# Kernel tuning notes

Measured on AMD Instinct MI355X. Metric: run time of the kernel, lower is better.

## Reference

```python
import jax, jax.numpy as jnp
import numpy as np

N, E, F, H, G = 50000, 1600000, 128, 128, 64
EPS = 1e-5  # BatchNorm eps


def setup_inputs() -> dict:
    key = jax.random.key(0)
    ks = jax.random.split(key, 16)
    x = jax.random.normal(ks[0], (N, F), dtype=jnp.float32)
    edge_index = jax.random.randint(ks[1], (2, E), 0, N, dtype=jnp.int64)
    batch = jnp.sort(jax.random.randint(ks[2], (N,), 0, G, dtype=jnp.int64))
    inp = {
        'x': x, 'edge_index': edge_index, 'batch': batch,
        'W1': jax.random.normal(ks[3], (F, H), dtype=jnp.float32) / np.sqrt(F),
        'b1': jnp.zeros((H,), jnp.float32),
        'bn1_gamma': jax.random.uniform(ks[4], (H,), jnp.float32, 0.5, 1.5),
        'bn1_beta': jax.random.normal(ks[5], (H,), jnp.float32) * 0.1,
        'bn1_mean': jax.random.normal(ks[6], (H,), jnp.float32) * 0.1,
        'bn1_var': jax.random.uniform(ks[7], (H,), jnp.float32, 0.5, 1.5),
        'W2': jax.random.normal(ks[8], (H, H), dtype=jnp.float32) / np.sqrt(H),
        'b2': jnp.zeros((H,), jnp.float32),
        'bn2_gamma': jax.random.uniform(ks[9], (H,), jnp.float32, 0.5, 1.5),
        'bn2_beta': jax.random.normal(ks[10], (H,), jnp.float32) * 0.1,
        'bn2_mean': jax.random.normal(ks[11], (H,), jnp.float32) * 0.1,
        'bn2_var': jax.random.uniform(ks[12], (H,), jnp.float32, 0.5, 1.5),
        'att_w': jax.random.normal(ks[13], (H, 1), dtype=jnp.float32) / np.sqrt(H),
        'cls_w': jax.random.normal(ks[14], (1, H), dtype=jnp.float32) / np.sqrt(H),
        'cls_b': jnp.zeros((1,), jnp.float32),
    }
    return inp


def gcn_conv(h, W, b, src, dst, n):
    # PyG GCNConv: linear, add self-loops, symmetric D^{-1/2}(A+I)D^{-1/2} aggregation, bias.
    hw = h @ W                                   # [n, H]
    loops = jnp.arange(n, dtype=src.dtype)
    s = jnp.concatenate([src, loops])
    d = jnp.concatenate([dst, loops])
    deg = jax.ops.segment_sum(jnp.ones_like(d, dtype=hw.dtype), d, num_segments=n)
    dis = jnp.where(deg > 0, jax.lax.rsqrt(deg), 0.0)
    norm = dis[s] * dis[d]                       # [E+n]
    msgs = hw[s] * norm[:, None]                 # gather + scale (memory-bound)
    return jax.ops.segment_sum(msgs, d, num_segments=n) + b


def batch_norm(h, gamma, beta, mean, var):
    return (h - mean) * gamma * jax.lax.rsqrt(var + EPS) + beta


def reference(x, edge_index, batch, W1, b1, bn1_gamma, bn1_beta, bn1_mean, bn1_var,
              W2, b2, bn2_gamma, bn2_beta, bn2_mean, bn2_var, att_w, cls_w, cls_b):
    n = x.shape[0]
    src, dst = edge_index[0], edge_index[1]
    # eval mode: dropout and edge-dropout are no-ops; BN uses running stats
    h = gcn_conv(x, W1, b1, src, dst, n)
    h = jax.nn.relu(batch_norm(h, bn1_gamma, bn1_beta, bn1_mean, bn1_var))
    h = gcn_conv(h, W2, b2, src, dst, n)
    h = jax.nn.relu(batch_norm(h, bn2_gamma, bn2_beta, bn2_mean, bn2_var))
    att = jax.nn.sigmoid(h @ att_w)              # [n, 1]
    g = jax.ops.segment_sum(h * att, batch, num_segments=G)  # [G, H]
    logits = g @ cls_w.T + cls_b                 # [G, 1]
    return logits, att
```

## Files before the change

kernel.cpp:

```cpp
#include <hip/hip_runtime.h>
#include <math.h>

#define NN 50000
#define HID 128
#define NG 64
#define BN_EPS 1e-5f

typedef __attribute__((ext_vector_type(8))) short short8;
typedef __attribute__((ext_vector_type(4))) float f32x4;

__device__ inline unsigned pack_bf2(float a, float b) {
    union { float f; unsigned u; } ua, ub;
    ua.f = a; ub.f = b;
    unsigned x = ua.u, y = ub.u;
    x += 0x7fffu + ((x >> 16) & 1u);
    y += 0x7fffu + ((y >> 16) & 1u);
    return (x >> 16) | (y & 0xffff0000u);
}
__device__ inline unsigned short bf16_1(float x) {
    union { float f; unsigned u; } v;
    v.f = x;
    unsigned r = v.u + 0x7fffu + ((v.u >> 16) & 1u);
    return (unsigned short)(r >> 16);
}
__device__ inline float2 unpack_bf2(unsigned v) {
    union { unsigned u; float f; } a, b;
    a.u = v << 16;
    b.u = v & 0xffff0000u;
    return make_float2(a.f, b.f);
}

#define NBKT 256
#define ETILE 2048
#define EPT   (ETILE / 256)
#define CAP   8192
#define ASTR 136

__global__ __launch_bounds__(128) void k_prep0(const float* __restrict__ W1,
                                               const float* __restrict__ W2,
                                               unsigned short* __restrict__ wt1,
                                               unsigned short* __restrict__ wt2,
                                               int* __restrict__ bcurP,
                                               const float* __restrict__ cls_b,
                                               float* __restrict__ logits) {
    int b = blockIdx.x;
    int t = threadIdx.x;
    if (b < 256) {
        int k = b & 127;
        const float* W = (b < 128) ? W1 : W2;
        unsigned short* wt = (b < 128) ? wt1 : wt2;
        wt[t * 128 + k] = bf16_1(W[k * 128 + t]);
    } else {
        #pragma unroll
        for (int i = 0; i < 32; ++i) bcurP[t * 32 + i] = 0;
        if (t < NG) logits[t] = cls_b[0];
    }
}

__global__ __launch_bounds__(256) void k_distribute(const int* __restrict__ src,
                                                    const int* __restrict__ dst,
                                                    int* __restrict__ bcurP,
                                                    unsigned* __restrict__ bpacked,
                                                    int E, int K) {
    __shared__ int h[NBKT];
    __shared__ int sx[NBKT];
    __shared__ int cur[NBKT];
    __shared__ int gb[NBKT];
    __shared__ unsigned stage[ETILE];
    int t = threadIdx.x;
    h[t] = 0;
    __syncthreads();
    int base = blockIdx.x * ETILE;
    int dreg[EPT];
    #pragma unroll
    for (int i = 0; i < EPT; ++i) {
        int e = base + i * 256 + t;
        dreg[i] = (e < E) ? dst[e] : -1;
        if (dreg[i] >= 0) atomicAdd(&h[dreg[i] / K], 1);
    }
    __syncthreads();
    int c = h[t];
    sx[t] = c;
    __syncthreads();
    for (int off = 1; off < NBKT; off <<= 1) {
        int v = (t >= off) ? sx[t - off] : 0;
        __syncthreads();
        sx[t] += v;
        __syncthreads();
    }
    int nvalid = sx[NBKT - 1];
    int excl = sx[t] - c;
    __syncthreads();
    sx[t] = excl;
    cur[t] = excl;
    gb[t] = (c > 0) ? atomicAdd(&bcurP[t * 16], c) : 0;
    __syncthreads();
    #pragma unroll
    for (int i = 0; i < EPT; ++i) {
        int e = base + i * 256 + t;
        if (dreg[i] >= 0) {
            int d = dreg[i];
            int bkt = d / K;
            int p = atomicAdd(&cur[bkt], 1);
            stage[p] = ((unsigned)d << 16) | (unsigned)src[e];
        }
    }
    __syncthreads();
    for (int idx = t; idx < nvalid; idx += 256) {
        unsigned v = stage[idx];
        int bkt = (int)(v >> 16) / K;
        int pos = gb[bkt] + (idx - sx[bkt]);
        bpacked[(size_t)bkt * CAP + pos] = v;
    }
}

__global__ __launch_bounds__(256) void k_csr_gemm1(const unsigned* __restrict__ bpacked,
                                                   const int* __restrict__ bcurP,
                                                   int* __restrict__ row_ptr,
                                                   int* __restrict__ degA,
                                                   float* __restrict__ dis,
                                                   int* __restrict__ col_idx,
                                                   const float* __restrict__ x,
                                                   const unsigned short* __restrict__ wt1,
                                                   unsigned short* __restrict__ zb,
                                                   int n, int K) {
    __shared__ unsigned short A[64][ASTR];
    __shared__ int cnt[NBKT];
    __shared__ int sA[NBKT];
    __shared__ int cur[NBKT];
    int t = threadIdx.x;
    int b = blockIdx.x;

    if (b >= NBKT) {
        int row0 = (b - NBKT) * 64;
        #pragma unroll
        for (int i = 0; i < 8; ++i) {
            int idx = t + i * 256;
            int r = idx >> 5;
            int c4 = (idx & 31) * 4;
            float4 v = make_float4(0.f, 0.f, 0.f, 0.f);
            if (row0 + r < n) v = *(const float4*)&x[(size_t)(row0 + r) * 128 + c4];
            uint2 p;
            p.x = pack_bf2(v.x, v.y);
            p.y = pack_bf2(v.z, v.w);
            *(uint2*)&A[r][c4] = p;
        }
        __syncthreads();
        int lane = t & 63;
        int wave = t >> 6;
        int m = lane & 15;
        int quad = lane >> 4;
        int r0 = wave * 16;
        short8 a[4];
        #pragma unroll
        for (int kt = 0; kt < 4; ++kt)
            a[kt] = *(const short8*)&A[r0 + m][kt * 32 + quad * 8];
        f32x4 acc[8];
        #pragma unroll
        for (int ct = 0; ct < 8; ++ct) acc[ct] = (f32x4){0.f, 0.f, 0.f, 0.f};
        short8 bcur[4], bnxt[4];
        {
            const unsigned short* wb = &wt1[(size_t)m * 128 + quad * 8];
            #pragma unroll
            for (int kt = 0; kt < 4; ++kt) bcur[kt] = *(const short8*)(wb + kt * 32);
        }
        #pragma unroll
        for (int ct = 0; ct < 8; ++ct) {
            if (ct < 7) {
                const unsigned short* wb = &wt1[(size_t)((ct + 1) * 16 + m) * 128 + quad * 8];
                #pragma unroll
                for (int kt = 0; kt < 4; ++kt) bnxt[kt] = *(const short8*)(wb + kt * 32);
            }
            #pragma unroll
            for (int kt = 0; kt < 4; ++kt)
                acc[ct] = __builtin_amdgcn_mfma_f32_16x16x32_bf16(a[kt], bcur[kt], acc[ct], 0, 0, 0);
            #pragma unroll
            for (int kt = 0; kt < 4; ++kt) bcur[kt] = bnxt[kt];
        }
        __syncthreads();
        #pragma unroll
        for (int ct = 0; ct < 8; ++ct) {
            int col = ct * 16 + m;
            #pragma unroll
            for (int reg = 0; reg < 4; ++reg)
                A[r0 + quad * 4 + reg][col] = bf16_1(acc[ct][reg]);
        }
        __syncthreads();
        #pragma unroll
        for (int i = 0; i < 4; ++i) {
            int idx = t + i * 256;
            int r = idx >> 4;
            int c8 = (idx & 15) * 8;
            int grow = row0 + r;
            if (grow < n)
                *(uint4*)&zb[(size_t)grow * 128 + c8] = *(const uint4*)&A[r][c8];
        }
        return;
    }

    int node0 = b * K;
    int nn = n - node0;
    if (nn > K) nn = K;
    if (nn < 0) nn = 0;
    int e0 = b * CAP;
    int e1 = e0 + bcurP[b * 16];
    cnt[t] = 0;
    __syncthreads();
    for (int e = e0 + t; e < e1; e += 256) {
        int ld = (int)(bpacked[e] >> 16) - node0;
        atomicAdd(&cnt[ld], 1);
    }
    __syncthreads();
    int c = cnt[t];
    sA[t] = c;
    __syncthreads();
    for (int off = 1; off < NBKT; off <<= 1) {
        int v = (t >= off) ? sA[t - off] : 0;
        __syncthreads();
        sA[t] += v;
        __syncthreads();
    }
    int rp = e0 + sA[t] - c;
    cur[t] = rp;
    if (t < nn) {
        row_ptr[node0 + t] = rp;
        degA[node0 + t] = c;
        dis[node0 + t] = rsqrtf((float)(c + 1));
    }
    __syncthreads();
    for (int e = e0 + t; e < e1; e += 256) {
        unsigned v = bpacked[e];
        int ld = (int)(v >> 16) - node0;
        int p = atomicAdd(&cur[ld], 1);
        col_idx[p] = (int)(v & 0xFFFFu);
    }
}

__global__ __launch_bounds__(256) void k_scale(unsigned short* __restrict__ zb,
                                               const float* __restrict__ dis, int n) {
    int i = blockIdx.x * 256 + threadIdx.x;
    int r = i >> 4;
    if (r >= n) return;
    int c8 = (i & 15) * 8;
    float s = dis[r];
    uint4 v = *(const uint4*)&zb[(size_t)r * 128 + c8];
    unsigned* w = (unsigned*)&v;
    #pragma unroll
    for (int k = 0; k < 4; ++k) {
        float2 f = unpack_bf2(w[k]);
        w[k] = pack_bf2(f.x * s, f.y * s);
    }
    *(uint4*)&zb[(size_t)r * 128 + c8] = v;
}


__device__ __forceinline__ void gather_pipe(const unsigned short* __restrict__ hws,
                                            const int* __restrict__ col_idx,
                                            int e0, int deg, int md, int sl, int part,
                                            float* acc8) {
    int nt = (md + 7) >> 3;
    if (nt <= 0) return;
    int base = part << 4;
    uint4 vA[8], vB[8];
    int c0, c1, n0 = 0, n1 = 0;
    c0 = (sl < deg) ? col_idx[e0 + sl] : 0;
    c1 = (sl + 16 < deg) ? col_idx[e0 + 16 + sl] : 0;

    #pragma unroll
    for (int j = 0; j < 8; ++j) {
        int s = __shfl(c0, base + j);
        vA[j] = (j < deg) ? *(const uint4*)(hws + ((size_t)s << 7) + (sl << 3))
                          : make_uint4(0, 0, 0, 0);
    }
    int t = 0, ebase = 0;
    for (;;) {
        if (t + 4 < nt) {
            n0 = (ebase + 32 + sl < deg) ? col_idx[e0 + ebase + 32 + sl] : 0;
            n1 = (ebase + 48 + sl < deg) ? col_idx[e0 + ebase + 48 + sl] : 0;
        }
        if (t + 1 < nt) {
            int it0 = (t + 1) << 3;
            #pragma unroll
            for (int j = 0; j < 8; ++j) {
                int s = __shfl(c0, base + 8 + j);
                vB[j] = (it0 + j < deg) ? *(const uint4*)(hws + ((size_t)s << 7) + (sl << 3))
                                        : make_uint4(0, 0, 0, 0);
            }
        }
        #pragma unroll
        for (int j = 0; j < 8; ++j) {
            const unsigned* w = (const unsigned*)&vA[j];
            #pragma unroll
            for (int i2 = 0; i2 < 4; ++i2) {
                float2 f = unpack_bf2(w[i2]);
                acc8[2 * i2]     += f.x;
                acc8[2 * i2 + 1] += f.y;
            }
        }
        if (++t >= nt) break;
        if (t + 1 < nt) {
            int it0 = (t + 1) << 3;
            #pragma unroll
            for (int j = 0; j < 8; ++j) {
                int s = __shfl(c1, base + j);
                vA[j] = (it0 + j < deg) ? *(const uint4*)(hws + ((size_t)s << 7) + (sl << 3))
                                        : make_uint4(0, 0, 0, 0);
            }
        }
        #pragma unroll
        for (int j = 0; j < 8; ++j) {
            const unsigned* w = (const unsigned*)&vB[j];
            #pragma unroll
            for (int i2 = 0; i2 < 4; ++i2) {
                float2 f = unpack_bf2(w[i2]);
                acc8[2 * i2]     += f.x;
                acc8[2 * i2 + 1] += f.y;
            }
        }
        if (++t >= nt) break;
        if (t + 1 < nt) {
            int it0 = (t + 1) << 3;
            #pragma unroll
            for (int j = 0; j < 8; ++j) {
                int s = __shfl(c1, base + 8 + j);
                vB[j] = (it0 + j < deg) ? *(const uint4*)(hws + ((size_t)s << 7) + (sl << 3))
                                        : make_uint4(0, 0, 0, 0);
            }
        }
        #pragma unroll
        for (int j = 0; j < 8; ++j) {
            const unsigned* w = (const unsigned*)&vA[j];
            #pragma unroll
            for (int i2 = 0; i2 < 4; ++i2) {
                float2 f = unpack_bf2(w[i2]);
                acc8[2 * i2]     += f.x;
                acc8[2 * i2 + 1] += f.y;
            }
        }
        if (++t >= nt) break;
        if (t + 1 < nt) {
            int it0 = (t + 1) << 3;
            #pragma unroll
            for (int j = 0; j < 8; ++j) {
                int s = __shfl(n0, base + j);
                vA[j] = (it0 + j < deg) ? *(const uint4*)(hws + ((size_t)s << 7) + (sl << 3))
                                        : make_uint4(0, 0, 0, 0);
            }
        }
        #pragma unroll
        for (int j = 0; j < 8; ++j) {
            const unsigned* w = (const unsigned*)&vB[j];
            #pragma unroll
            for (int i2 = 0; i2 < 4; ++i2) {
                float2 f = unpack_bf2(w[i2]);
                acc8[2 * i2]     += f.x;
                acc8[2 * i2 + 1] += f.y;
            }
        }
        if (++t >= nt) break;
        c0 = n0; c1 = n1; ebase += 32;
    }
}


__global__ __launch_bounds__(256, 3) void k_agg1_gemm2(const unsigned short* __restrict__ zb,
                                                       const int* __restrict__ row_ptr,
                                                       const int* __restrict__ degA,
                                                       const int* __restrict__ col_idx,
                                                       const float* __restrict__ dis,
                                                       const float* __restrict__ bias,
                                                       const float* __restrict__ gamma,
                                                       const float* __restrict__ beta,
                                                       const float* __restrict__ mean,
                                                       const float* __restrict__ var,
                                                       const unsigned short* __restrict__ wt2,
                                                       unsigned short* __restrict__ hwsb2, int n) {
    __shared__ unsigned short H1[16][ASTR];
    __shared__ unsigned short C2[16][ASTR];
    int t = threadIdx.x;
    int wave = t >> 6, lane = t & 63;
    int sl = lane & 15, part = lane >> 4;
    int d = blockIdx.x * 16 + wave * 4 + part;
    bool active = (d < n);
    int e0 = 0, deg = 0;
    if (active) {
        e0 = row_ptr[d];
        deg = degA[d];
    }
    uint4 vs = make_uint4(0, 0, 0, 0);
    float dd = 0.f;
    if (active) {
        vs = *(const uint4*)(zb + ((size_t)d << 7) + (sl << 3));
        dd = dis[d];
    }
    int md = deg;
    md = max(md, __shfl_xor(md, 16));
    md = max(md, __shfl_xor(md, 32));

    float acc8[8] = {0, 0, 0, 0, 0, 0, 0, 0};
    gather_pipe(zb, col_idx, e0, deg, md, sl, part, acc8);

    unsigned outw[4] = {0, 0, 0, 0};
    if (active) {
        const unsigned* w = (const unsigned*)&vs;
        #pragma unroll
        for (int i2 = 0; i2 < 4; ++i2) {
            float2 f = unpack_bf2(w[i2]);
            acc8[2 * i2]     += f.x;
            acc8[2 * i2 + 1] += f.y;
        }
        int f0 = sl << 3;
        #pragma unroll
        for (int i2 = 0; i2 < 4; ++i2) {
            int f = f0 + 2 * i2;
            float2 bv = *(const float2*)&bias[f];
            float2 gm = *(const float2*)&gamma[f];
            float2 bt = *(const float2*)&beta[f];
            float2 mn = *(const float2*)&mean[f];
            float2 vr = *(const float2*)&var[f];
            float vx = acc8[2 * i2] * dd + bv.x;
            float vy = acc8[2 * i2 + 1] * dd + bv.y;
            float sx = gm.x * rsqrtf(vr.x + BN_EPS);
            float sy = gm.y * rsqrtf(vr.y + BN_EPS);
            float rx = fmaxf((vx - mn.x) * sx + bt.x, 0.f);
            float ry = fmaxf((vy - mn.y) * sy + bt.y, 0.f);
            outw[i2] = pack_bf2(rx, ry);
        }
    }
    int local = wave * 4 + part;
    *(uint4*)&H1[local][sl << 3] = *(uint4*)outw;
    __syncthreads();

    int m = sl;
    int quad = part;
    short8 a2[4];
    #pragma unroll
    for (int kt = 0; kt < 4; ++kt)
        a2[kt] = *(const short8*)&H1[m][kt * 32 + quad * 8];

    f32x4 acc2[2];
    acc2[0] = (f32x4){0.f, 0.f, 0.f, 0.f};
    acc2[1] = (f32x4){0.f, 0.f, 0.f, 0.f};
    #pragma unroll
    for (int i = 0; i < 2; ++i) {
        int ct = wave * 2 + i;
        const unsigned short* wb = &wt2[(size_t)(ct * 16 + m) * 128 + quad * 8];
        #pragma unroll
        for (int kt = 0; kt < 4; ++kt) {
            short8 b = *(const short8*)(wb + kt * 32);
            acc2[i] = __builtin_amdgcn_mfma_f32_16x16x32_bf16(a2[kt], b, acc2[i], 0, 0, 0);
        }
    }
    int gr = blockIdx.x * 16 + quad * 4;
    float ds2[4];
    #pragma unroll
    for (int reg = 0; reg < 4; ++reg)
        ds2[reg] = (gr + reg < n) ? dis[gr + reg] : 0.f;
    #pragma unroll
    for (int i = 0; i < 2; ++i) {
        int col = (wave * 2 + i) * 16 + m;
        #pragma unroll
        for (int reg = 0; reg < 4; ++reg)
            C2[quad * 4 + reg][col] = bf16_1(acc2[i][reg] * ds2[reg]);
    }
    __syncthreads();
    {
        int r = t >> 4;
        int c8 = (t & 15) * 8;
        int grow = blockIdx.x * 16 + r;
        if (grow < n)
            *(uint4*)&hwsb2[(size_t)grow * 128 + c8] = *(const uint4*)&C2[r][c8];
    }
}


__global__ __launch_bounds__(256, 3) void k_agg2_att_logit(const unsigned short* __restrict__ hwsb,
                                                           const int* __restrict__ row_ptr,
                                                           const int* __restrict__ degA,
                                                           const int* __restrict__ col_idx,
                                                           const float* __restrict__ dis,
                                                           const float* __restrict__ bias,
                                                           const float* __restrict__ gamma,
                                                           const float* __restrict__ beta,
                                                           const float* __restrict__ mean,
                                                           const float* __restrict__ var,
                                                           const int* __restrict__ batch,
                                                           const float* __restrict__ att_w,
                                                           const float* __restrict__ cls_w,
                                                           float* __restrict__ att_out,
                                                           float* __restrict__ logits, int n) {
    __shared__ int   sg[16];
    __shared__ float sv[16];
    int t = threadIdx.x;
    int wave = t >> 6, lane = t & 63;
    int sl = lane & 15, part = lane >> 4;
    int d = blockIdx.x * 16 + wave * 4 + part;
    bool active = (d < n);
    int e0 = 0, deg = 0;
    if (active) {
        e0 = row_ptr[d];
        deg = degA[d];
    }
    uint4 vs = make_uint4(0, 0, 0, 0);
    float dd = 0.f;
    int g = -1;
    if (active) {
        vs = *(const uint4*)(hwsb + ((size_t)d << 7) + (sl << 3));
        dd = dis[d];
        g = batch[d];
    }
    int md = deg;
    md = max(md, __shfl_xor(md, 16));
    md = max(md, __shfl_xor(md, 32));

    float acc8[8] = {0, 0, 0, 0, 0, 0, 0, 0};
    gather_pipe(hwsb, col_idx, e0, deg, md, sl, part, acc8);

    float contrib = 0.f;
    float p = 0.f, q = 0.f;
    if (active) {
        const unsigned* w = (const unsigned*)&vs;
        #pragma unroll
        for (int i2 = 0; i2 < 4; ++i2) {
            float2 f = unpack_bf2(w[i2]);
            acc8[2 * i2]     += f.x;
            acc8[2 * i2 + 1] += f.y;
        }
        int f0 = sl << 3;
        #pragma unroll
        for (int i2 = 0; i2 < 4; ++i2) {
            int f = f0 + 2 * i2;
            float2 bv = *(const float2*)&bias[f];
            float2 gm = *(const float2*)&gamma[f];
            float2 bt = *(const float2*)&beta[f];
            float2 mn = *(const float2*)&mean[f];
            float2 vr = *(const float2*)&var[f];
            float vx = acc8[2 * i2] * dd + bv.x;
            float vy = acc8[2 * i2 + 1] * dd + bv.y;
            float sx = gm.x * rsqrtf(vr.x + BN_EPS);
            float sy = gm.y * rsqrtf(vr.y + BN_EPS);
            float rx = fmaxf((vx - mn.x) * sx + bt.x, 0.f);
            float ry = fmaxf((vy - mn.y) * sy + bt.y, 0.f);
            float2 aw = *(const float2*)&att_w[f];
            float2 cw = *(const float2*)&cls_w[f];
            p += rx * aw.x + ry * aw.y;
            q += rx * cw.x + ry * cw.y;
        }
    }
    #pragma unroll
    for (int off = 1; off < 16; off <<= 1) {
        p += __shfl_xor(p, off);
        q += __shfl_xor(q, off);
    }
    if (active) {
        float a = 1.f / (1.f + expf(-p));
        if (sl == 0) att_out[d] = a;
        contrib = a * q;
    }
    if (sl == 0) {
        sg[wave * 4 + part] = g;
        sv[wave * 4 + part] = contrib;
    }
    __syncthreads();
    if (t == 0) {
        int cur = -1;
        float acc = 0.f;
        #pragma unroll
        for (int i = 0; i < 16; ++i) {
            int gi = sg[i];
            if (gi < 0) continue;
            if (gi != cur) {
                if (cur >= 0) atomicAdd(&logits[cur], acc);
                cur = gi;
                acc = 0.f;
            }
            acc += sv[i];
        }
        if (cur >= 0) atomicAdd(&logits[cur], acc);
    }
}


extern "C" void kernel_launch(void* const* d_in, const int* in_sizes, int n_in,
                              void* d_out, int out_size, void* d_ws, size_t ws_size,
                              hipStream_t stream) {
    const float* x   = (const float*)d_in[0];
    const int*   ei  = (const int*)d_in[1];
    const int*   bat = (const int*)d_in[2];
    const float* W1  = (const float*)d_in[3];
    const float* b1  = (const float*)d_in[4];
    const float* g1  = (const float*)d_in[5];
    const float* bt1 = (const float*)d_in[6];
    const float* mn1 = (const float*)d_in[7];
    const float* vr1 = (const float*)d_in[8];
    const float* W2  = (const float*)d_in[9];
    const float* b2  = (const float*)d_in[10];
    const float* g2  = (const float*)d_in[11];
    const float* bt2 = (const float*)d_in[12];
    const float* mn2 = (const float*)d_in[13];
    const float* vr2 = (const float*)d_in[14];
    const float* attw = (const float*)d_in[15];
    const float* clsw = (const float*)d_in[16];
    const float* clsb = (const float*)d_in[17];

    int E = in_sizes[1] / 2;
    int n = in_sizes[2];
    const int* src = ei;
    const int* dst = ei + E;
    int K = (n + NBKT - 1) / NBKT;

    char* ws = (char*)d_ws;
    auto alloc = [&](size_t bytes) {
        void* p = (void*)ws;
        ws += (bytes + 255) & ~(size_t)255;
        return p;
    };
    int*            bcurP   = (int*)alloc(NBKT * 16 * 4);
    unsigned*       bpacked = (unsigned*)alloc((size_t)NBKT * CAP * 4);
    int*            row_ptr = (int*)alloc((size_t)n * 4);
    int*            degA    = (int*)alloc((size_t)n * 4);
    int*            col_idx = (int*)alloc(((size_t)NBKT * CAP + 1024) * 4);
    float*          dis     = (float*)alloc((size_t)n * 4);
    unsigned short* zb      = (unsigned short*)alloc((size_t)n * 128 * 2);
    unsigned short* hwsb2   = (unsigned short*)alloc((size_t)n * 128 * 2);
    unsigned short* wt1     = (unsigned short*)alloc(128 * 128 * 2);
    unsigned short* wt2     = (unsigned short*)alloc(128 * 128 * 2);

    float* out = (float*)d_out;
    int etiles = (E + ETILE - 1) / ETILE;
    int gb = (n + 63) / 64;
    int ab = (n + 15) / 16;
    int sb = (n * 16 + 255) / 256;

    k_prep0<<<257, 128, 0, stream>>>(W1, W2, wt1, wt2, bcurP, clsb, out);
    k_distribute<<<etiles, 256, 0, stream>>>(src, dst, bcurP, bpacked, E, K);
    k_csr_gemm1<<<NBKT + gb, 256, 0, stream>>>(bpacked, bcurP, row_ptr, degA, dis,
                                               col_idx, x, wt1, zb, n, K);
    k_scale<<<sb, 256, 0, stream>>>(zb, dis, n);
    k_agg1_gemm2<<<ab, 256, 0, stream>>>(zb, row_ptr, degA, col_idx, dis,
                                         b1, g1, bt1, mn1, vr1, wt2, hwsb2, n);
    k_agg2_att_logit<<<ab, 256, 0, stream>>>(hwsb2, row_ptr, degA, col_idx, dis,
                                             b2, g2, bt2, mn2, vr2, bat, attw, clsw,
                                             out + NG, out, n);
}
```

Before: 279.6 us.

## Fuse edge distribution with GEMM1, scale into CSR build, use 16-bit column indices

Moves the first dense GEMM out of the CSR-build kernel and into the edge-distribute kernel as extra blocks. The CSR build now also applies the D^-1/2 row scaling to the GEMM output, which removes the separate scale kernel. Column indices are stored as 16-bit values staged through shared memory, halving index traffic in both gather passes. The edge tile size doubles and bpacked is read with vector loads. Risks: 16-bit indices only work while n fits in 65536, and the larger tile raises shared-memory use per distribute block.

```diff
diff --git a/kernel.cpp b/kernel.cpp
--- a/kernel.cpp
+++ b/kernel.cpp
@@ -31,7 +31,7 @@
 }
 
 #define NBKT 256
-#define ETILE 2048
+#define ETILE 4096
 #define EPT   (ETILE / 256)
 #define CAP   8192
 #define ASTR 136
@@ -57,158 +57,170 @@
     }
 }
 
-__global__ __launch_bounds__(256) void k_distribute(const int* __restrict__ src,
+struct SmemDist {
+    int h[NBKT], sx[NBKT], cur[NBKT], gb[NBKT];
+    unsigned stage[ETILE];
+};
+
+__global__ __launch_bounds__(256) void k_dist_gemm1(const int* __restrict__ src,
                                                     const int* __restrict__ dst,
                                                     int* __restrict__ bcurP,
                                                     unsigned* __restrict__ bpacked,
-                                                    int E, int K) {
-    __shared__ int h[NBKT];
-    __shared__ int sx[NBKT];
-    __shared__ int cur[NBKT];
-    __shared__ int gb[NBKT];
-    __shared__ unsigned stage[ETILE];
+                                                    const float* __restrict__ x,
+                                                    const unsigned short* __restrict__ wt1,
+                                                    unsigned short* __restrict__ zb,
+                                                    int E, int K, int n, int DB) {
+    __shared__ __align__(16) char smem[sizeof(SmemDist)];
     int t = threadIdx.x;
-    h[t] = 0;
-    __syncthreads();
-    int base = blockIdx.x * ETILE;
-    int dreg[EPT];
-    #pragma unroll
-    for (int i = 0; i < EPT; ++i) {
-        int e = base + i * 256 + t;
-        dreg[i] = (e < E) ? dst[e] : -1;
-        if (dreg[i] >= 0) atomicAdd(&h[dreg[i] / K], 1);
-    }
-    __syncthreads();
-    int c = h[t];
-    sx[t] = c;
-    __syncthreads();
-    for (int off = 1; off < NBKT; off <<= 1) {
-        int v = (t >= off) ? sx[t - off] : 0;
-        __syncthreads();
-        sx[t] += v;
-        __syncthreads();
-    }
-    int nvalid = sx[NBKT - 1];
-    int excl = sx[t] - c;
-    __syncthreads();
-    sx[t] = excl;
-    cur[t] = excl;
-    gb[t] = (c > 0) ? atomicAdd(&bcurP[t * 16], c) : 0;
-    __syncthreads();
-    #pragma unroll
-    for (int i = 0; i < EPT; ++i) {
-        int e = base + i * 256 + t;
-        if (dreg[i] >= 0) {
-            int d = dreg[i];
-            int bkt = d / K;
-            int p = atomicAdd(&cur[bkt], 1);
-            stage[p] = ((unsigned)d << 16) | (unsigned)src[e];
-        }
-    }
-    __syncthreads();
-    for (int idx = t; idx < nvalid; idx += 256) {
-        unsigned v = stage[idx];
-        int bkt = (int)(v >> 16) / K;
-        int pos = gb[bkt] + (idx - sx[bkt]);
-        bpacked[(size_t)bkt * CAP + pos] = v;
-    }
-}
-
-__global__ __launch_bounds__(256) void k_csr_gemm1(const unsigned* __restrict__ bpacked,
+    int b = blockIdx.x;
+
+    if (b < DB) {
+        SmemDist* s = (SmemDist*)smem;
+        s->h[t] = 0;
+        __syncthreads();
+        int base = b * ETILE;
+        int dreg[EPT];
+        #pragma unroll
+        for (int i = 0; i < EPT; ++i) {
+            int e = base + i * 256 + t;
+            dreg[i] = (e < E) ? dst[e] : -1;
+            if (dreg[i] >= 0) atomicAdd(&s->h[dreg[i] / K], 1);
+        }
+        __syncthreads();
+        int c = s->h[t];
+        s->sx[t] = c;
+        __syncthreads();
+        for (int off = 1; off < NBKT; off <<= 1) {
+            int v = (t >= off) ? s->sx[t - off] : 0;
+            __syncthreads();
+            s->sx[t] += v;
+            __syncthreads();
+        }
+        int nvalid = s->sx[NBKT - 1];
+        int excl = s->sx[t] - c;
+        __syncthreads();
+        s->sx[t] = excl;
+        s->cur[t] = excl;
+        s->gb[t] = (c > 0) ? atomicAdd(&bcurP[t * 16], c) : 0;
+        __syncthreads();
+        #pragma unroll
+        for (int i = 0; i < EPT; ++i) {
+            int e = base + i * 256 + t;
+            if (dreg[i] >= 0) {
+                int d = dreg[i];
+                int bkt = d / K;
+                int p = atomicAdd(&s->cur[bkt], 1);
+                s->stage[p] = ((unsigned)d << 16) | (unsigned)src[e];
+            }
+        }
+        __syncthreads();
+        for (int idx = t; idx < nvalid; idx += 256) {
+            unsigned v = s->stage[idx];
+            int bkt = (int)(v >> 16) / K;
+            int pos = s->gb[bkt] + (idx - s->sx[bkt]);
+            bpacked[(size_t)bkt * CAP + pos] = v;
+        }
+        return;
+    }
+
+    typedef unsigned short ArowT[ASTR];
+    ArowT* A = (ArowT*)smem;
+    int row0 = (b - DB) * 64;
+    #pragma unroll
+    for (int i = 0; i < 8; ++i) {
+        int idx = t + i * 256;
+        int r = idx >> 5;
+        int c4 = (idx & 31) * 4;
+        float4 v = make_float4(0.f, 0.f, 0.f, 0.f);
+        if (row0 + r < n) v = *(const float4*)&x[(size_t)(row0 + r) * 128 + c4];
+        uint2 p;
+        p.x = pack_bf2(v.x, v.y);
+        p.y = pack_bf2(v.z, v.w);
+        *(uint2*)&A[r][c4] = p;
+    }
+    __syncthreads();
+    int lane = t & 63;
+    int wave = t >> 6;
+    int m = lane & 15;
+    int quad = lane >> 4;
+    int r0 = wave * 16;
+    short8 a[4];
+    #pragma unroll
+    for (int kt = 0; kt < 4; ++kt)
+        a[kt] = *(const short8*)&A[r0 + m][kt * 32 + quad * 8];
+    f32x4 acc[8];
+    #pragma unroll
+    for (int ct = 0; ct < 8; ++ct) acc[ct] = (f32x4){0.f, 0.f, 0.f, 0.f};
+    short8 bcur[4], bnxt[4];
+    {
+        const unsigned short* wb = &wt1[(size_t)m * 128 + quad * 8];
+        #pragma unroll
+        for (int kt = 0; kt < 4; ++kt) bcur[kt] = *(const short8*)(wb + kt * 32);
+    }
+    #pragma unroll
+    for (int ct = 0; ct < 8; ++ct) {
+        if (ct < 7) {
+            const unsigned short* wb = &wt1[(size_t)((ct + 1) * 16 + m) * 128 + quad * 8];
+            #pragma unroll
+            for (int kt = 0; kt < 4; ++kt) bnxt[kt] = *(const short8*)(wb + kt * 32);
+        }
+        #pragma unroll
+        for (int kt = 0; kt < 4; ++kt)
+            acc[ct] = __builtin_amdgcn_mfma_f32_16x16x32_bf16(a[kt], bcur[kt], acc[ct], 0, 0, 0);
+        #pragma unroll
+        for (int kt = 0; kt < 4; ++kt) bcur[kt] = bnxt[kt];
+    }
+    __syncthreads();
+    #pragma unroll
+    for (int ct = 0; ct < 8; ++ct) {
+        int col = ct * 16 + m;
+        #pragma unroll
+        for (int reg = 0; reg < 4; ++reg)
+            A[r0 + quad * 4 + reg][col] = bf16_1(acc[ct][reg]);
+    }
+    __syncthreads();
+    #pragma unroll
+    for (int i = 0; i < 4; ++i) {
+        int idx = t + i * 256;
+        int r = idx >> 4;
+        int c8 = (idx & 15) * 8;
+        int grow = row0 + r;
+        if (grow < n)
+            *(uint4*)&zb[(size_t)grow * 128 + c8] = *(const uint4*)&A[r][c8];
+    }
+}
+
+__global__ __launch_bounds__(256) void k_csr_scale(const unsigned* __restrict__ bpacked,
                                                    const int* __restrict__ bcurP,
                                                    int* __restrict__ row_ptr,
                                                    int* __restrict__ degA,
                                                    float* __restrict__ dis,
-                                                   int* __restrict__ col_idx,
-                                                   const float* __restrict__ x,
-                                                   const unsigned short* __restrict__ wt1,
+                                                   unsigned short* __restrict__ col16,
                                                    unsigned short* __restrict__ zb,
                                                    int n, int K) {
-    __shared__ unsigned short A[64][ASTR];
     __shared__ int cnt[NBKT];
     __shared__ int sA[NBKT];
     __shared__ int cur[NBKT];
+    __shared__ float disL[NBKT];
+    __shared__ unsigned short stage[CAP];
     int t = threadIdx.x;
     int b = blockIdx.x;
-
-    if (b >= NBKT) {
-        int row0 = (b - NBKT) * 64;
-        #pragma unroll
-        for (int i = 0; i < 8; ++i) {
-            int idx = t + i * 256;
-            int r = idx >> 5;
-            int c4 = (idx & 31) * 4;
-            float4 v = make_float4(0.f, 0.f, 0.f, 0.f);
-            if (row0 + r < n) v = *(const float4*)&x[(size_t)(row0 + r) * 128 + c4];
-            uint2 p;
-            p.x = pack_bf2(v.x, v.y);
-            p.y = pack_bf2(v.z, v.w);
-            *(uint2*)&A[r][c4] = p;
-        }
-        __syncthreads();
-        int lane = t & 63;
-        int wave = t >> 6;
-        int m = lane & 15;
-        int quad = lane >> 4;
-        int r0 = wave * 16;
-        short8 a[4];
-        #pragma unroll
-        for (int kt = 0; kt < 4; ++kt)
-            a[kt] = *(const short8*)&A[r0 + m][kt * 32 + quad * 8];
-        f32x4 acc[8];
-        #pragma unroll
-        for (int ct = 0; ct < 8; ++ct) acc[ct] = (f32x4){0.f, 0.f, 0.f, 0.f};
-        short8 bcur[4], bnxt[4];
-        {
-            const unsigned short* wb = &wt1[(size_t)m * 128 + quad * 8];
-            #pragma unroll
-            for (int kt = 0; kt < 4; ++kt) bcur[kt] = *(const short8*)(wb + kt * 32);
-        }
-        #pragma unroll
-        for (int ct = 0; ct < 8; ++ct) {
-            if (ct < 7) {
-                const unsigned short* wb = &wt1[(size_t)((ct + 1) * 16 + m) * 128 + quad * 8];
-                #pragma unroll
-                for (int kt = 0; kt < 4; ++kt) bnxt[kt] = *(const short8*)(wb + kt * 32);
-            }
-            #pragma unroll
-            for (int kt = 0; kt < 4; ++kt)
-                acc[ct] = __builtin_amdgcn_mfma_f32_16x16x32_bf16(a[kt], bcur[kt], acc[ct], 0, 0, 0);
-            #pragma unroll
-            for (int kt = 0; kt < 4; ++kt) bcur[kt] = bnxt[kt];
-        }
-        __syncthreads();
-        #pragma unroll
-        for (int ct = 0; ct < 8; ++ct) {
-            int col = ct * 16 + m;
-            #pragma unroll
-            for (int reg = 0; reg < 4; ++reg)
-                A[r0 + quad * 4 + reg][col] = bf16_1(acc[ct][reg]);
-        }
-        __syncthreads();
-        #pragma unroll
-        for (int i = 0; i < 4; ++i) {
-            int idx = t + i * 256;
-            int r = idx >> 4;
-            int c8 = (idx & 15) * 8;
-            int grow = row0 + r;
-            if (grow < n)
-                *(uint4*)&zb[(size_t)grow * 128 + c8] = *(const uint4*)&A[r][c8];
-        }
-        return;
-    }
-
     int node0 = b * K;
     int nn = n - node0;
     if (nn > K) nn = K;
     if (nn < 0) nn = 0;
     int e0 = b * CAP;
-    int e1 = e0 + bcurP[b * 16];
+    int ne = bcurP[b * 16];
     cnt[t] = 0;
     __syncthreads();
-    for (int e = e0 + t; e < e1; e += 256) {
-        int ld = (int)(bpacked[e] >> 16) - node0;
-        atomicAdd(&cnt[ld], 1);
+    int n4 = (ne + 3) >> 2;
+    for (int i = t; i < n4; i += 256) {
+        uint4 v = *(const uint4*)&bpacked[e0 + 4 * i];
+        int rem = ne - 4 * i;
+        if (rem > 0) atomicAdd(&cnt[(int)(v.x >> 16) - node0], 1);
+        if (rem > 1) atomicAdd(&cnt[(int)(v.y >> 16) - node0], 1);
+        if (rem > 2) atomicAdd(&cnt[(int)(v.z >> 16) - node0], 1);
+        if (rem > 3) atomicAdd(&cnt[(int)(v.w >> 16) - node0], 1);
     }
     __syncthreads();
     int c = cnt[t];
@@ -220,42 +232,54 @@
         sA[t] += v;
         __syncthreads();
     }
-    int rp = e0 + sA[t] - c;
-    cur[t] = rp;
+    int excl = sA[t] - c;
+    cur[t] = excl;
+    float dv = rsqrtf((float)(c + 1));
+    disL[t] = dv;
     if (t < nn) {
-        row_ptr[node0 + t] = rp;
+        row_ptr[node0 + t] = e0 + excl;
         degA[node0 + t] = c;
-        dis[node0 + t] = rsqrtf((float)(c + 1));
-    }
-    __syncthreads();
-    for (int e = e0 + t; e < e1; e += 256) {
-        unsigned v = bpacked[e];
-        int ld = (int)(v >> 16) - node0;
-        int p = atomicAdd(&cur[ld], 1);
-        col_idx[p] = (int)(v & 0xFFFFu);
-    }
-}
-
-__global__ __launch_bounds__(256) void k_scale(unsigned short* __restrict__ zb,
-                                               const float* __restrict__ dis, int n) {
-    int i = blockIdx.x * 256 + threadIdx.x;
-    int r = i >> 4;
-    if (r >= n) return;
-    int c8 = (i & 15) * 8;
-    float s = dis[r];
-    uint4 v = *(const uint4*)&zb[(size_t)r * 128 + c8];
-    unsigned* w = (unsigned*)&v;
-    #pragma unroll
-    for (int k = 0; k < 4; ++k) {
-        float2 f = unpack_bf2(w[k]);
-        w[k] = pack_bf2(f.x * s, f.y * s);
-    }
-    *(uint4*)&zb[(size_t)r * 128 + c8] = v;
+        dis[node0 + t] = dv;
+    }
+    __syncthreads();
+    for (int i = t; i < n4; i += 256) {
+        uint4 v = *(const uint4*)&bpacked[e0 + 4 * i];
+        int rem = ne - 4 * i;
+        unsigned vv[4] = {v.x, v.y, v.z, v.w};
+        #pragma unroll
+        for (int j = 0; j < 4; ++j) {
+            if (rem > j) {
+                int ld = (int)(vv[j] >> 16) - node0;
+                int p = atomicAdd(&cur[ld], 1);
+                stage[p] = (unsigned short)(vv[j] & 0xFFFFu);
+            }
+        }
+    }
+    __syncthreads();
+    int nw = (ne + 1) >> 1;
+    for (int i = t; i < nw; i += 256) {
+        unsigned w = (unsigned)stage[2 * i] | ((unsigned)stage[2 * i + 1] << 16);
+        *(unsigned*)&col16[e0 + 2 * i] = w;
+    }
+    for (int idx = t; idx < nn * 16; idx += 256) {
+        int r = idx >> 4;
+        int c8 = (idx & 15) * 8;
+        float sc = disL[r];
+        size_t o8 = (size_t)(node0 + r) * 128 + c8;
+        uint4 v = *(const uint4*)&zb[o8];
+        unsigned* w = (unsigned*)&v;
+        #pragma unroll
+        for (int k2 = 0; k2 < 4; ++k2) {
+            float2 f = unpack_bf2(w[k2]);
+            w[k2] = pack_bf2(f.x * sc, f.y * sc);
+        }
+        *(uint4*)&zb[o8] = v;
+    }
 }
 
 
 __device__ __forceinline__ void gather_pipe(const unsigned short* __restrict__ hws,
-                                            const int* __restrict__ col_idx,
+                                            const unsigned short* __restrict__ col16,
                                             int e0, int deg, int md, int sl, int part,
                                             float* acc8) {
     int nt = (md + 7) >> 3;
@@ -263,8 +287,8 @@
     int base = part << 4;
     uint4 vA[8], vB[8];
     int c0, c1, n0 = 0, n1 = 0;
-    c0 = (sl < deg) ? col_idx[e0 + sl] : 0;
-    c1 = (sl + 16 < deg) ? col_idx[e0 + 16 + sl] : 0;
+    c0 = (sl < deg) ? (int)col16[e0 + sl] : 0;
+    c1 = (sl + 16 < deg) ? (int)col16[e0 + 16 + sl] : 0;
 
     #pragma unroll
     for (int j = 0; j < 8; ++j) {
@@ -275,8 +299,8 @@
     int t = 0, ebase = 0;
     for (;;) {
         if (t + 4 < nt) {
-            n0 = (ebase + 32 + sl < deg) ? col_idx[e0 + ebase + 32 + sl] : 0;
-            n1 = (ebase + 48 + sl < deg) ? col_idx[e0 + ebase + 48 + sl] : 0;
+            n0 = (ebase + 32 + sl < deg) ? (int)col16[e0 + ebase + 32 + sl] : 0;
+            n1 = (ebase + 48 + sl < deg) ? (int)col16[e0 + ebase + 48 + sl] : 0;
         }
         if (t + 1 < nt) {
             int it0 = (t + 1) << 3;
@@ -366,7 +390,7 @@
 __global__ __launch_bounds__(256, 3) void k_agg1_gemm2(const unsigned short* __restrict__ zb,
                                                        const int* __restrict__ row_ptr,
                                                        const int* __restrict__ degA,
-                                                       const int* __restrict__ col_idx,
+                                                       const unsigned short* __restrict__ col16,
                                                        const float* __restrict__ dis,
                                                        const float* __restrict__ bias,
                                                        const float* __restrict__ gamma,
@@ -398,7 +422,7 @@
     md = max(md, __shfl_xor(md, 32));
 
     float acc8[8] = {0, 0, 0, 0, 0, 0, 0, 0};
-    gather_pipe(zb, col_idx, e0, deg, md, sl, part, acc8);
+    gather_pipe(zb, col16, e0, deg, md, sl, part, acc8);
 
     unsigned outw[4] = {0, 0, 0, 0};
     if (active) {
@@ -477,7 +501,7 @@
 __global__ __launch_bounds__(256, 3) void k_agg2_att_logit(const unsigned short* __restrict__ hwsb,
                                                            const int* __restrict__ row_ptr,
                                                            const int* __restrict__ degA,
-                                                           const int* __restrict__ col_idx,
+                                                           const unsigned short* __restrict__ col16,
                                                            const float* __restrict__ dis,
                                                            const float* __restrict__ bias,
                                                            const float* __restrict__ gamma,
@@ -514,7 +538,7 @@
     md = max(md, __shfl_xor(md, 32));
 
     float acc8[8] = {0, 0, 0, 0, 0, 0, 0, 0};
-    gather_pipe(hwsb, col_idx, e0, deg, md, sl, part, acc8);
+    gather_pipe(hwsb, col16, e0, deg, md, sl, part, acc8);
 
     float contrib = 0.f;
     float p = 0.f, q = 0.f;
@@ -619,7 +643,7 @@
     unsigned*       bpacked = (unsigned*)alloc((size_t)NBKT * CAP * 4);
     int*            row_ptr = (int*)alloc((size_t)n * 4);
     int*            degA    = (int*)alloc((size_t)n * 4);
-    int*            col_idx = (int*)alloc(((size_t)NBKT * CAP + 1024) * 4);
+    unsigned short* col16   = (unsigned short*)alloc(((size_t)NBKT * CAP + 1024) * 2);
     float*          dis     = (float*)alloc((size_t)n * 4);
     unsigned short* zb      = (unsigned short*)alloc((size_t)n * 128 * 2);
     unsigned short* hwsb2   = (unsigned short*)alloc((size_t)n * 128 * 2);
@@ -627,19 +651,18 @@
     unsigned short* wt2     = (unsigned short*)alloc(128 * 128 * 2);
 
     float* out = (float*)d_out;
-    int etiles = (E + ETILE - 1) / ETILE;
+    int DB = (E + ETILE - 1) / ETILE;
     int gb = (n + 63) / 64;
     int ab = (n + 15) / 16;
-    int sb = (n * 16 + 255) / 256;
 
     k_prep0<<<257, 128, 0, stream>>>(W1, W2, wt1, wt2, bcurP, clsb, out);
-    k_distribute<<<etiles, 256, 0, stream>>>(src, dst, bcurP, bpacked, E, K);
-    k_csr_gemm1<<<NBKT + gb, 256, 0, stream>>>(bpacked, bcurP, row_ptr, degA, dis,
-                                               col_idx, x, wt1, zb, n, K);
-    k_scale<<<sb, 256, 0, stream>>>(zb, dis, n);
-    k_agg1_gemm2<<<ab, 256, 0, stream>>>(zb, row_ptr, degA, col_idx, dis,
+    k_dist_gemm1<<<DB + gb, 256, 0, stream>>>(src, dst, bcurP, bpacked, x, wt1, zb,
+                                              E, K, n, DB);
+    k_csr_scale<<<NBKT, 256, 0, stream>>>(bpacked, bcurP, row_ptr, degA, dis,
+                                          col16, zb, n, K);
+    k_agg1_gemm2<<<ab, 256, 0, stream>>>(zb, row_ptr, degA, col16, dis,
                                          b1, g1, bt1, mn1, vr1, wt2, hwsb2, n);
-    k_agg2_att_logit<<<ab, 256, 0, stream>>>(hwsb2, row_ptr, degA, col_idx, dis,
+    k_agg2_att_logit<<<ab, 256, 0, stream>>>(hwsb2, row_ptr, degA, col16, dis,
                                              b2, g2, bt2, mn2, vr2, bat, attw, clsw,
                                              out + NG, out, n);
 }
```

New measurement: 267.7 us. 1.04x faster.
